# Kernel tuning notes

Measured on AMD Instinct MI355X. Metric: run time of the kernel, lower is better.

Reference implementation:

```python
import jax, jax.numpy as jnp
import numpy as np

T, B, IN_DIM, H = 4096, 2048, 1, 10  # len(input), seq_length, input_dim, hidden_dim


def setup_inputs() -> dict:
    key = jax.random.key(0)
    ks = jax.random.split(key, 11)
    s_in = 1.0 / np.sqrt(H)  # torch LSTM/Linear init scale
    u = lambda k, shape: jax.random.uniform(k, shape, jnp.float32, -s_in, s_in)
    return {
        "x": jax.random.normal(ks[0], (T, B, IN_DIM), jnp.float32),
        # layer 0 (input_size=1), layer 1 (input_size=H); torch gate order i,f,g,o
        "W_ih0": u(ks[1], (4 * H, IN_DIM)),
        "W_hh0": u(ks[2], (4 * H, H)),
        "b_ih0": u(ks[3], (4 * H,)),
        "b_hh0": u(ks[4], (4 * H,)),
        "W_ih1": u(ks[5], (4 * H, H)),
        "W_hh1": u(ks[6], (4 * H, H)),
        "b_ih1": u(ks[7], (4 * H,)),
        "b_hh1": u(ks[8], (4 * H,)),
        "W_lin": u(ks[9], (1, H)),
        "b_lin": u(ks[10], (1,)),
    }


def _lstm_layer(x, W_ih, W_hh, b_ih, b_hh):
    # x: (T, B, in); precompute input contributions for all timesteps at once
    xw = jnp.einsum("tbi,gi->tbg", x, W_ih) + b_ih + b_hh  # (T, B, 4H)
    Whh_T = W_hh.T

    def step(carry, xt):
        h, c = carry
        gates = xt + h @ Whh_T  # (B, 4H)
        i, f, g, o = jnp.split(gates, 4, axis=-1)
        i = jax.nn.sigmoid(i)
        f = jax.nn.sigmoid(f)
        g = jnp.tanh(g)
        o = jax.nn.sigmoid(o)
        c = f * c + i * g
        h = o * jnp.tanh(c)
        return (h, c), h

    b = x.shape[1]
    h0 = jnp.zeros((b, W_hh.shape[1]), x.dtype)
    _, hs = jax.lax.scan(step, (h0, h0), xw)
    return hs  # (T, B, H)


def reference(x, W_ih0, W_hh0, b_ih0, b_hh0, W_ih1, W_hh1, b_ih1, b_hh1, W_lin, b_lin):
    h1 = _lstm_layer(x, W_ih0, W_hh0, b_ih0, b_hh0)   # (T, B, H)
    h2 = _lstm_layer(h1, W_ih1, W_hh1, b_ih1, b_hh1)  # (T, B, H)
    # faithful to original: view(seq_length, len(input), H)[-1] is a raw reshape
    last = h2.reshape(B, T, H)[-1]                    # (T, H)
    return last @ W_lin.T + b_lin                     # (T, 1)
```

## Files before the change

### kernel.cpp

```cpp
#include <hip/hip_runtime.h>

namespace {

constexpr int T_STEPS = 4096;
constexpr int NBATCH  = 2048;
constexpr int HID     = 10;
constexpr float L2E   = 1.4426950408889634f;

typedef float v2f __attribute__((ext_vector_type(2)));
typedef float v4f __attribute__((ext_vector_type(4)));

__device__ __forceinline__ float ex2(float x){ return __builtin_amdgcn_exp2f(x); }
__device__ __forceinline__ float rcp_(float x){ return __builtin_amdgcn_rcpf(x); }

template<int IMM>
__device__ __forceinline__ float swz(float v){
    return __int_as_float(__builtin_amdgcn_ds_swizzle(__float_as_int(v), IMM));
}
__device__ __forceinline__ float bperm(int addr, float v){
    return __int_as_float(__builtin_amdgcn_ds_bpermute(addr, __float_as_int(v)));
}
template<int CTRL>
__device__ __forceinline__ float dpp(float v){
    return __int_as_float(__builtin_amdgcn_update_dpp(0, __float_as_int(v), CTRL, 0xF, 0xF, true));
}
__device__ __forceinline__ void pk_fma(v2f &a, v2f b, v2f c){
    asm("v_pk_fma_f32 %0, %1, %2, %0" : "+v"(a) : "v"(b), "v"(c));
}


__device__ __forceinline__ void lstm_step(
    const v2f (&Wp)[2][5], float wx0, float wx1, float b0, float b1,
    float selA, float kA, float kB,
    float* hwp, const char* rdb,
    float &hn, float &c, float xv,
    float wlin, float blin, int t_l1, float* __restrict__ out, int b)
{
    *hwp = hn;
    asm volatile("" ::: "memory");
    const v4f Va = *(const v4f*)(rdb);
    const v4f Vb = *(const v4f*)(rdb+16);
    const v2f Vc = *(const v2f*)(rdb+32);
    const v2f va01 = __builtin_shufflevector(Va, Va, 0, 1);
    const v2f va23 = __builtin_shufflevector(Va, Va, 2, 3);
    const v2f vb01 = __builtin_shufflevector(Vb, Vb, 0, 1);
    const v2f vb23 = __builtin_shufflevector(Vb, Vb, 2, 3);

    v2f A0 = { fmaf(wx0, xv, b0), 0.0f };
    v2f A1 = { fmaf(wx1, xv, b1), 0.0f };
    pk_fma(A0, Wp[0][0], va01);  pk_fma(A1, Wp[1][0], va01);
    pk_fma(A0, Wp[0][1], va23);  pk_fma(A1, Wp[1][1], va23);
    pk_fma(A0, Wp[0][2], vb01);  pk_fma(A1, Wp[1][2], vb01);
    pk_fma(A0, Wp[0][3], vb23);  pk_fma(A1, Wp[1][3], vb23);
    pk_fma(A0, Wp[0][4], Vc);    pk_fma(A1, Wp[1][4], Vc);
    float a0 = A0.x + A0.y;
    float a1 = A1.x + A1.y;

    a0 = fmaf(selA, dpp<0x108>(a0), a0);
    a1 = fmaf(selA, dpp<0x108>(a1), a1);

    const float r0 = rcp_(1.0f + ex2(a0));
    const float r1 = rcp_(1.0f + ex2(a1));
    const float g0 = fmaf(kA, r0, kB);
    const float g1 = r1;

    const float gv = dpp<0x101>(g0);
    const float ov = dpp<0x101>(g1);
    c = fmaf(g1, c, g0 * gv);
    const float tc = fmaf(-2.0f, rcp_(1.0f + ex2(c * (2.0f*L2E))), 1.0f);
    hn = ov * tc;

    if (t_l1 >= T_STEPS-2) {
        float p = hn * wlin;
        p += swz<0x041F>(p); p += swz<0x081F>(p); p += swz<0x101F>(p);
        p += swz<0x201F>(p); p += swz<0x401F>(p);
        p += bperm((((int)threadIdx.x ^ 32) & 63)*4, p);
        if (threadIdx.x == 0)
            out[(t_l1 - (T_STEPS-2))*NBATCH + b] = p + blin;
    }
}

__device__ __forceinline__ float rdlane(float v, int lane){
    return __int_as_float(__builtin_amdgcn_readlane(__float_as_int(v), lane));
}

__global__ __launch_bounds__(64) void lstm2_kernel(
    const float* __restrict__ x,
    const float* __restrict__ Wih0, const float* __restrict__ Whh0,
    const float* __restrict__ bih0, const float* __restrict__ bhh0,
    const float* __restrict__ Wih1, const float* __restrict__ Whh1,
    const float* __restrict__ bih1, const float* __restrict__ bhh1,
    const float* __restrict__ Wlin, const float* __restrict__ blin_p,
    float* __restrict__ out)
{
    __shared__ float hx[96];

    const int tid = (int)threadIdx.x;
    const int b   = (int)blockIdx.x;

    int role, q;
    if      (tid < 16){ role=0; q=tid; }
    else if (tid < 24){ role=1; q=tid-16; }
    else if (tid < 32){ role=2; q=tid-24; }
    else if (tid < 40){ role=1; q=tid-32+8; }
    else if (tid < 48){ role=2; q=tid-40+8; }
    else if (tid < 52){ role=1; q=tid-48+16; }
    else if (tid < 56){ role=0; q=tid-52+16; }
    else if (tid < 60){ role=2; q=tid-56+16; }
    else              { role=3; q=0; }
    const int h = q >> 1, p = q & 1;
    const int gate0 = p ? 2 : 0, gate1 = p ? 3 : 1;
    const float s0 = (gate0 == 2) ? 2.0f*L2E : -L2E;
    const float s1 = -L2E;

    float W0[HID], W1[HID], wx0=0.0f, wx1=0.0f, b0=0.0f, b1=0.0f;
    const int r0i = gate0*HID + h, r1i = gate1*HID + h;
    if (role == 0){
        #pragma unroll
        for (int j=0;j<HID;++j){ W0[j]=Whh0[r0i*HID+j]*s0; W1[j]=Whh0[r1i*HID+j]*s1; }
        wx0 = Wih0[r0i]*s0;  wx1 = Wih0[r1i]*s1;
        b0 = (bih0[r0i]+bhh0[r0i])*s0;  b1 = (bih0[r1i]+bhh0[r1i])*s1;
    } else if (role == 1){
        #pragma unroll
        for (int j=0;j<HID;++j){ W0[j]=Wih1[r0i*HID+j]*s0; W1[j]=Wih1[r1i*HID+j]*s1; }
        b0 = (bih1[r0i]+bhh1[r0i])*s0;  b1 = (bih1[r1i]+bhh1[r1i])*s1;
    } else if (role == 2){
        #pragma unroll
        for (int j=0;j<HID;++j){ W0[j]=Whh1[r0i*HID+j]*s0; W1[j]=Whh1[r1i*HID+j]*s1; }
    } else {
        #pragma unroll
        for (int j=0;j<HID;++j){ W0[j]=0.0f; W1[j]=0.0f; }
    }
    v2f Wp[2][5];
    #pragma unroll
    for (int k=0;k<5;++k){ Wp[0][k]=v2f{W0[2*k],W0[2*k+1]}; Wp[1][k]=v2f{W1[2*k],W1[2*k+1]}; }

    const float selA = (role==1) ? 1.0f : 0.0f;
    const float kA = p ? -2.0f : 1.0f;
    const float kB = p ?  1.0f : 0.0f;
    const bool owner = (p==0) && (role==0 || role==1);
    const int wslot = owner ? (role==0 ? h : 12+h) : (24+tid);
    float* hwp = &hx[wslot];
    const char* rdb = (const char*)hx + (role==2 ? 48 : 0);
    const float wlin = (role==1 && p==0) ? Wlin[h] : 0.0f;
    const float blin = blin_p[0];

    float hn = 0.0f, c = 0.0f;

    const float* xp = x + (size_t)(tid & 7) * NBATCH + b;
    float xpre = xp[0];

    {
        const float zb0 = (role==0) ? b0 : 0.0f, zb1 = (role==0) ? b1 : 0.0f;
        lstm_step(Wp, wx0,wx1, zb0,zb1, selA,kA,kB, hwp,rdb, hn,c, rdlane(xpre,0), wlin,blin, -1, out, b);
        lstm_step(Wp, wx0,wx1, b0,b1, selA,kA,kB, hwp,rdb, hn,c, rdlane(xpre,1), wlin,blin, 0, out, b);
        lstm_step(Wp, wx0,wx1, b0,b1, selA,kA,kB, hwp,rdb, hn,c, rdlane(xpre,2), wlin,blin, 1, out, b);
        lstm_step(Wp, wx0,wx1, b0,b1, selA,kA,kB, hwp,rdb, hn,c, rdlane(xpre,3), wlin,blin, 2, out, b);
        lstm_step(Wp, wx0,wx1, b0,b1, selA,kA,kB, hwp,rdb, hn,c, rdlane(xpre,4), wlin,blin, 3, out, b);
        lstm_step(Wp, wx0,wx1, b0,b1, selA,kA,kB, hwp,rdb, hn,c, rdlane(xpre,5), wlin,blin, 4, out, b);
        lstm_step(Wp, wx0,wx1, b0,b1, selA,kA,kB, hwp,rdb, hn,c, rdlane(xpre,6), wlin,blin, 5, out, b);
        lstm_step(Wp, wx0,wx1, b0,b1, selA,kA,kB, hwp,rdb, hn,c, rdlane(xpre,7), wlin,blin, 6, out, b);
    }

    for (int i=1; i<512; ++i){
        const float xcur = xp[(size_t)i*8*NBATCH];
        const int s0b = i*8;
        lstm_step(Wp, wx0,wx1, b0,b1, selA,kA,kB, hwp,rdb, hn,c, rdlane(xcur,0), wlin,blin, s0b-1, out, b);
        lstm_step(Wp, wx0,wx1, b0,b1, selA,kA,kB, hwp,rdb, hn,c, rdlane(xcur,1), wlin,blin, s0b+0, out, b);
        lstm_step(Wp, wx0,wx1, b0,b1, selA,kA,kB, hwp,rdb, hn,c, rdlane(xcur,2), wlin,blin, s0b+1, out, b);
        lstm_step(Wp, wx0,wx1, b0,b1, selA,kA,kB, hwp,rdb, hn,c, rdlane(xcur,3), wlin,blin, s0b+2, out, b);
        lstm_step(Wp, wx0,wx1, b0,b1, selA,kA,kB, hwp,rdb, hn,c, rdlane(xcur,4), wlin,blin, s0b+3, out, b);
        lstm_step(Wp, wx0,wx1, b0,b1, selA,kA,kB, hwp,rdb, hn,c, rdlane(xcur,5), wlin,blin, s0b+4, out, b);
        lstm_step(Wp, wx0,wx1, b0,b1, selA,kA,kB, hwp,rdb, hn,c, rdlane(xcur,6), wlin,blin, s0b+5, out, b);
        lstm_step(Wp, wx0,wx1, b0,b1, selA,kA,kB, hwp,rdb, hn,c, rdlane(xcur,7), wlin,blin, s0b+6, out, b);
    }

    lstm_step(Wp, wx0,wx1, b0,b1, selA,kA,kB, hwp,rdb, hn,c, 0.0f, wlin,blin, T_STEPS-1, out, b);
}

}

extern "C" void kernel_launch(void* const* d_in, const int* in_sizes, int n_in,
                              void* d_out, int out_size, void* d_ws, size_t ws_size,
                              hipStream_t stream) {
    const float* x    = (const float*)d_in[0];
    const float* Wih0 = (const float*)d_in[1];
    const float* Whh0 = (const float*)d_in[2];
    const float* bih0 = (const float*)d_in[3];
    const float* bhh0 = (const float*)d_in[4];
    const float* Wih1 = (const float*)d_in[5];
    const float* Whh1 = (const float*)d_in[6];
    const float* bih1 = (const float*)d_in[7];
    const float* bhh1 = (const float*)d_in[8];
    const float* Wlin = (const float*)d_in[9];
    const float* blin = (const float*)d_in[10];
    float* out = (float*)d_out;

    hipLaunchKernelGGL(lstm2_kernel, dim3(NBATCH), dim3(64), 0, stream,
                       x, Wih0, Whh0, bih0, bhh0, Wih1, Whh1, bih1, bhh1, Wlin, blin, out);
}
```

Before: 901.0 us.

## Double-buffer LDS hidden-state exchange and prefetch next x chunk one iteration ahead

Each step now writes its new hidden state into the LDS buffer that the following step reads, instead of writing the previous step's state at the start of the step. Even and odd steps alternate between two buffers, so the store can come right after the state is computed. This moves the LDS write off the front of each step's critical path and removes the read-after-write ordering within a step. The x input for the next group of 8 steps is also loaded one loop iteration early, hiding global-load latency. The cost is more LDS, an explicit zero-init of both buffers, and one extra live register.

```diff
diff --git a/kernel.cpp b/kernel.cpp
--- a/kernel.cpp
+++ b/kernel.cpp
@@ -26,6 +26,9 @@
 }
 __device__ __forceinline__ void pk_fma(v2f &a, v2f b, v2f c){
     asm("v_pk_fma_f32 %0, %1, %2, %0" : "+v"(a) : "v"(b), "v"(c));
+}
+__device__ __forceinline__ float rdlane(float v, int lane){
+    return __int_as_float(__builtin_amdgcn_readlane(__float_as_int(v), lane));
 }
 
 
@@ -36,8 +39,6 @@
     float &hn, float &c, float xv,
     float wlin, float blin, int t_l1, float* __restrict__ out, int b)
 {
-    *hwp = hn;
-    asm volatile("" ::: "memory");
     const v4f Va = *(const v4f*)(rdb);
     const v4f Vb = *(const v4f*)(rdb+16);
     const v2f Vc = *(const v2f*)(rdb+32);
@@ -70,6 +71,9 @@
     const float tc = fmaf(-2.0f, rcp_(1.0f + ex2(c * (2.0f*L2E))), 1.0f);
     hn = ov * tc;
 
+    *hwp = hn;
+    asm volatile("" ::: "memory");
+
     if (t_l1 >= T_STEPS-2) {
         float p = hn * wlin;
         p += swz<0x041F>(p); p += swz<0x081F>(p); p += swz<0x101F>(p);
@@ -78,10 +82,6 @@
         if (threadIdx.x == 0)
             out[(t_l1 - (T_STEPS-2))*NBATCH + b] = p + blin;
     }
-}
-
-__device__ __forceinline__ float rdlane(float v, int lane){
-    return __int_as_float(__builtin_amdgcn_readlane(__float_as_int(v), lane));
 }
 
 __global__ __launch_bounds__(64) void lstm2_kernel(
@@ -93,7 +93,7 @@
     const float* __restrict__ Wlin, const float* __restrict__ blin_p,
     float* __restrict__ out)
 {
-    __shared__ float hx[96];
+    __shared__ __attribute__((aligned(16))) float hx[128];
 
     const int tid = (int)threadIdx.x;
     const int b   = (int)blockIdx.x;
@@ -139,43 +139,52 @@
     const float kA = p ? -2.0f : 1.0f;
     const float kB = p ?  1.0f : 0.0f;
     const bool owner = (p==0) && (role==0 || role==1);
-    const int wslot = owner ? (role==0 ? h : 12+h) : (24+tid);
-    float* hwp = &hx[wslot];
-    const char* rdb = (const char*)hx + (role==2 ? 48 : 0);
+    const int slot = owner ? (role==0 ? h : 12+h) : -1;
+
+    float* hwpE = &hx[slot >= 0 ? 24+slot : 48+tid];
+    float* hwpO = &hx[slot >= 0 ?    slot : 48+tid];
+    const char* rdbE = (const char*)hx + (role==2 ? 48 : 0);
+    const char* rdbO = (const char*)hx + 96 + (role==2 ? 48 : 0);
     const float wlin = (role==1 && p==0) ? Wlin[h] : 0.0f;
     const float blin = blin_p[0];
 
+    hx[slot >= 0 ? slot : 48+tid] = 0.0f;
+    hx[slot >= 0 ? 24+slot : 48+tid] = 0.0f;
+    asm volatile("" ::: "memory");
+
     float hn = 0.0f, c = 0.0f;
 
     const float* xp = x + (size_t)(tid & 7) * NBATCH + b;
-    float xpre = xp[0];
+    float xcur = xp[0];
+    float xnxt = xp[(size_t)8 * NBATCH];
 
     {
         const float zb0 = (role==0) ? b0 : 0.0f, zb1 = (role==0) ? b1 : 0.0f;
-        lstm_step(Wp, wx0,wx1, zb0,zb1, selA,kA,kB, hwp,rdb, hn,c, rdlane(xpre,0), wlin,blin, -1, out, b);
-        lstm_step(Wp, wx0,wx1, b0,b1, selA,kA,kB, hwp,rdb, hn,c, rdlane(xpre,1), wlin,blin, 0, out, b);
-        lstm_step(Wp, wx0,wx1, b0,b1, selA,kA,kB, hwp,rdb, hn,c, rdlane(xpre,2), wlin,blin, 1, out, b);
-        lstm_step(Wp, wx0,wx1, b0,b1, selA,kA,kB, hwp,rdb, hn,c, rdlane(xpre,3), wlin,blin, 2, out, b);
-        lstm_step(Wp, wx0,wx1, b0,b1, selA,kA,kB, hwp,rdb, hn,c, rdlane(xpre,4), wlin,blin, 3, out, b);
-        lstm_step(Wp, wx0,wx1, b0,b1, selA,kA,kB, hwp,rdb, hn,c, rdlane(xpre,5), wlin,blin, 4, out, b);
-        lstm_step(Wp, wx0,wx1, b0,b1, selA,kA,kB, hwp,rdb, hn,c, rdlane(xpre,6), wlin,blin, 5, out, b);
-        lstm_step(Wp, wx0,wx1, b0,b1, selA,kA,kB, hwp,rdb, hn,c, rdlane(xpre,7), wlin,blin, 6, out, b);
+        lstm_step(Wp, wx0,wx1, zb0,zb1, selA,kA,kB, hwpE,rdbE, hn,c, rdlane(xcur,0), wlin,blin, -1, out, b);
+        lstm_step(Wp, wx0,wx1, b0,b1, selA,kA,kB, hwpO,rdbO, hn,c, rdlane(xcur,1), wlin,blin, 0, out, b);
+        lstm_step(Wp, wx0,wx1, b0,b1, selA,kA,kB, hwpE,rdbE, hn,c, rdlane(xcur,2), wlin,blin, 1, out, b);
+        lstm_step(Wp, wx0,wx1, b0,b1, selA,kA,kB, hwpO,rdbO, hn,c, rdlane(xcur,3), wlin,blin, 2, out, b);
+        lstm_step(Wp, wx0,wx1, b0,b1, selA,kA,kB, hwpE,rdbE, hn,c, rdlane(xcur,4), wlin,blin, 3, out, b);
+        lstm_step(Wp, wx0,wx1, b0,b1, selA,kA,kB, hwpO,rdbO, hn,c, rdlane(xcur,5), wlin,blin, 4, out, b);
+        lstm_step(Wp, wx0,wx1, b0,b1, selA,kA,kB, hwpE,rdbE, hn,c, rdlane(xcur,6), wlin,blin, 5, out, b);
+        lstm_step(Wp, wx0,wx1, b0,b1, selA,kA,kB, hwpO,rdbO, hn,c, rdlane(xcur,7), wlin,blin, 6, out, b);
     }
 
     for (int i=1; i<512; ++i){
-        const float xcur = xp[(size_t)i*8*NBATCH];
+        xcur = xnxt;
+        if (i < 511) xnxt = xp[(size_t)(i+1)*8*NBATCH];
         const int s0b = i*8;
-        lstm_step(Wp, wx0,wx1, b0,b1, selA,kA,kB, hwp,rdb, hn,c, rdlane(xcur,0), wlin,blin, s0b-1, out, b);
-        lstm_step(Wp, wx0,wx1, b0,b1, selA,kA,kB, hwp,rdb, hn,c, rdlane(xcur,1), wlin,blin, s0b+0, out, b);
-        lstm_step(Wp, wx0,wx1, b0,b1, selA,kA,kB, hwp,rdb, hn,c, rdlane(xcur,2), wlin,blin, s0b+1, out, b);
-        lstm_step(Wp, wx0,wx1, b0,b1, selA,kA,kB, hwp,rdb, hn,c, rdlane(xcur,3), wlin,blin, s0b+2, out, b);
-        lstm_step(Wp, wx0,wx1, b0,b1, selA,kA,kB, hwp,rdb, hn,c, rdlane(xcur,4), wlin,blin, s0b+3, out, b);
-        lstm_step(Wp, wx0,wx1, b0,b1, selA,kA,kB, hwp,rdb, hn,c, rdlane(xcur,5), wlin,blin, s0b+4, out, b);
-        lstm_step(Wp, wx0,wx1, b0,b1, selA,kA,kB, hwp,rdb, hn,c, rdlane(xcur,6), wlin,blin, s0b+5, out, b);
-        lstm_step(Wp, wx0,wx1, b0,b1, selA,kA,kB, hwp,rdb, hn,c, rdlane(xcur,7), wlin,blin, s0b+6, out, b);
-    }
-
-    lstm_step(Wp, wx0,wx1, b0,b1, selA,kA,kB, hwp,rdb, hn,c, 0.0f, wlin,blin, T_STEPS-1, out, b);
+        lstm_step(Wp, wx0,wx1, b0,b1, selA,kA,kB, hwpE,rdbE, hn,c, rdlane(xcur,0), wlin,blin, s0b-1, out, b);
+        lstm_step(Wp, wx0,wx1, b0,b1, selA,kA,kB, hwpO,rdbO, hn,c, rdlane(xcur,1), wlin,blin, s0b+0, out, b);
+        lstm_step(Wp, wx0,wx1, b0,b1, selA,kA,kB, hwpE,rdbE, hn,c, rdlane(xcur,2), wlin,blin, s0b+1, out, b);
+        lstm_step(Wp, wx0,wx1, b0,b1, selA,kA,kB, hwpO,rdbO, hn,c, rdlane(xcur,3), wlin,blin, s0b+2, out, b);
+        lstm_step(Wp, wx0,wx1, b0,b1, selA,kA,kB, hwpE,rdbE, hn,c, rdlane(xcur,4), wlin,blin, s0b+3, out, b);
+        lstm_step(Wp, wx0,wx1, b0,b1, selA,kA,kB, hwpO,rdbO, hn,c, rdlane(xcur,5), wlin,blin, s0b+4, out, b);
+        lstm_step(Wp, wx0,wx1, b0,b1, selA,kA,kB, hwpE,rdbE, hn,c, rdlane(xcur,6), wlin,blin, s0b+5, out, b);
+        lstm_step(Wp, wx0,wx1, b0,b1, selA,kA,kB, hwpO,rdbO, hn,c, rdlane(xcur,7), wlin,blin, s0b+6, out, b);
+    }
+
+    lstm_step(Wp, wx0,wx1, b0,b1, selA,kA,kB, hwpE,rdbE, hn,c, 0.0f, wlin,blin, T_STEPS-1, out, b);
 }
 
 }
```

After: 817.3 us. 9.3% less time.

## Restructure LSTM step: LDS exchange at step end, shared reciprocal, x prefetch

Applied to the files above, without the earlier changes.

Each step now writes the new hidden state to LDS and reads the neighbours' values at the end of the step, carrying them in registers into the next step. Four other changes come with it. The two sigmoid reciprocals are merged into one rcp of the product of the denominators. The x load is software-prefetched one 8-step block ahead. The output-reduction branch becomes a compile-time template flag. Non-owner write slots move to avoid overlapping the read window, and LDS is aligned and enlarged. These changes aim to shorten the serial dependency chain per timestep, at the risk of a small precision change from the combined reciprocal.

```diff
diff --git a/kernel.cpp b/kernel.cpp
--- a/kernel.cpp
+++ b/kernel.cpp
@@ -27,24 +27,25 @@
 __device__ __forceinline__ void pk_fma(v2f &a, v2f b, v2f c){
     asm("v_pk_fma_f32 %0, %1, %2, %0" : "+v"(a) : "v"(b), "v"(c));
 }
-
-
+__device__ __forceinline__ float rdlane(float v, int lane){
+    return __int_as_float(__builtin_amdgcn_readlane(__float_as_int(v), lane));
+}
+
+
+template<bool OUT>
 __device__ __forceinline__ void lstm_step(
     const v2f (&Wp)[2][5], float wx0, float wx1, float b0, float b1,
     float selA, float kA, float kB,
     float* hwp, const char* rdb,
+    v4f &Va, v4f &Vb, v2f &Vc,
     float &hn, float &c, float xv,
-    float wlin, float blin, int t_l1, float* __restrict__ out, int b)
+    float wlin, float blin, int t_l1, float* out, int b)
 {
-    *hwp = hn;
-    asm volatile("" ::: "memory");
-    const v4f Va = *(const v4f*)(rdb);
-    const v4f Vb = *(const v4f*)(rdb+16);
-    const v2f Vc = *(const v2f*)(rdb+32);
     const v2f va01 = __builtin_shufflevector(Va, Va, 0, 1);
     const v2f va23 = __builtin_shufflevector(Va, Va, 2, 3);
     const v2f vb01 = __builtin_shufflevector(Vb, Vb, 0, 1);
     const v2f vb23 = __builtin_shufflevector(Vb, Vb, 2, 3);
+    const v2f vc01 = Vc;
 
     v2f A0 = { fmaf(wx0, xv, b0), 0.0f };
     v2f A1 = { fmaf(wx1, xv, b1), 0.0f };
@@ -52,15 +53,18 @@
     pk_fma(A0, Wp[0][1], va23);  pk_fma(A1, Wp[1][1], va23);
     pk_fma(A0, Wp[0][2], vb01);  pk_fma(A1, Wp[1][2], vb01);
     pk_fma(A0, Wp[0][3], vb23);  pk_fma(A1, Wp[1][3], vb23);
-    pk_fma(A0, Wp[0][4], Vc);    pk_fma(A1, Wp[1][4], Vc);
+    pk_fma(A0, Wp[0][4], vc01);  pk_fma(A1, Wp[1][4], vc01);
     float a0 = A0.x + A0.y;
     float a1 = A1.x + A1.y;
 
     a0 = fmaf(selA, dpp<0x108>(a0), a0);
     a1 = fmaf(selA, dpp<0x108>(a1), a1);
 
-    const float r0 = rcp_(1.0f + ex2(a0));
-    const float r1 = rcp_(1.0f + ex2(a1));
+    const float e0 = ex2(a0), e1 = ex2(a1);
+    const float d0 = 1.0f + e0, d1 = 1.0f + e1;
+    const float rD = rcp_(d0 * d1);
+    const float r0 = d1 * rD;
+    const float r1 = d0 * rD;
     const float g0 = fmaf(kA, r0, kB);
     const float g1 = r1;
 
@@ -70,7 +74,13 @@
     const float tc = fmaf(-2.0f, rcp_(1.0f + ex2(c * (2.0f*L2E))), 1.0f);
     hn = ov * tc;
 
-    if (t_l1 >= T_STEPS-2) {
+    *hwp = hn;
+    asm volatile("" ::: "memory");
+    Va = *(const v4f*)(rdb);
+    Vb = *(const v4f*)(rdb+16);
+    Vc = *(const v2f*)(rdb+32);
+
+    if (OUT) {
         float p = hn * wlin;
         p += swz<0x041F>(p); p += swz<0x081F>(p); p += swz<0x101F>(p);
         p += swz<0x201F>(p); p += swz<0x401F>(p);
@@ -78,10 +88,6 @@
         if (threadIdx.x == 0)
             out[(t_l1 - (T_STEPS-2))*NBATCH + b] = p + blin;
     }
-}
-
-__device__ __forceinline__ float rdlane(float v, int lane){
-    return __int_as_float(__builtin_amdgcn_readlane(__float_as_int(v), lane));
 }
 
 __global__ __launch_bounds__(64) void lstm2_kernel(
@@ -93,7 +99,7 @@
     const float* __restrict__ Wlin, const float* __restrict__ blin_p,
     float* __restrict__ out)
 {
-    __shared__ float hx[96];
+    __shared__ __attribute__((aligned(16))) float hx[112];
 
     const int tid = (int)threadIdx.x;
     const int b   = (int)blockIdx.x;
@@ -139,43 +145,58 @@
     const float kA = p ? -2.0f : 1.0f;
     const float kB = p ?  1.0f : 0.0f;
     const bool owner = (p==0) && (role==0 || role==1);
-    const int wslot = owner ? (role==0 ? h : 12+h) : (24+tid);
+    const int wslot = owner ? (role==0 ? h : 12+h) : (48+tid);
     float* hwp = &hx[wslot];
     const char* rdb = (const char*)hx + (role==2 ? 48 : 0);
     const float wlin = (role==1 && p==0) ? Wlin[h] : 0.0f;
     const float blin = blin_p[0];
 
     float hn = 0.0f, c = 0.0f;
+    v4f Va = {0,0,0,0}, Vb = {0,0,0,0};
+    v2f Vc = {0,0};
 
     const float* xp = x + (size_t)(tid & 7) * NBATCH + b;
-    float xpre = xp[0];
+    float xcur = xp[0];
+    float xnxt = xp[(size_t)8 * NBATCH];
 
     {
         const float zb0 = (role==0) ? b0 : 0.0f, zb1 = (role==0) ? b1 : 0.0f;
-        lstm_step(Wp, wx0,wx1, zb0,zb1, selA,kA,kB, hwp,rdb, hn,c, rdlane(xpre,0), wlin,blin, -1, out, b);
-        lstm_step(Wp, wx0,wx1, b0,b1, selA,kA,kB, hwp,rdb, hn,c, rdlane(xpre,1), wlin,blin, 0, out, b);
-        lstm_step(Wp, wx0,wx1, b0,b1, selA,kA,kB, hwp,rdb, hn,c, rdlane(xpre,2), wlin,blin, 1, out, b);
-        lstm_step(Wp, wx0,wx1, b0,b1, selA,kA,kB, hwp,rdb, hn,c, rdlane(xpre,3), wlin,blin, 2, out, b);
-        lstm_step(Wp, wx0,wx1, b0,b1, selA,kA,kB, hwp,rdb, hn,c, rdlane(xpre,4), wlin,blin, 3, out, b);
-        lstm_step(Wp, wx0,wx1, b0,b1, selA,kA,kB, hwp,rdb, hn,c, rdlane(xpre,5), wlin,blin, 4, out, b);
-        lstm_step(Wp, wx0,wx1, b0,b1, selA,kA,kB, hwp,rdb, hn,c, rdlane(xpre,6), wlin,blin, 5, out, b);
-        lstm_step(Wp, wx0,wx1, b0,b1, selA,kA,kB, hwp,rdb, hn,c, rdlane(xpre,7), wlin,blin, 6, out, b);
-    }
-
-    for (int i=1; i<512; ++i){
-        const float xcur = xp[(size_t)i*8*NBATCH];
-        const int s0b = i*8;
-        lstm_step(Wp, wx0,wx1, b0,b1, selA,kA,kB, hwp,rdb, hn,c, rdlane(xcur,0), wlin,blin, s0b-1, out, b);
-        lstm_step(Wp, wx0,wx1, b0,b1, selA,kA,kB, hwp,rdb, hn,c, rdlane(xcur,1), wlin,blin, s0b+0, out, b);
-        lstm_step(Wp, wx0,wx1, b0,b1, selA,kA,kB, hwp,rdb, hn,c, rdlane(xcur,2), wlin,blin, s0b+1, out, b);
-        lstm_step(Wp, wx0,wx1, b0,b1, selA,kA,kB, hwp,rdb, hn,c, rdlane(xcur,3), wlin,blin, s0b+2, out, b);
-        lstm_step(Wp, wx0,wx1, b0,b1, selA,kA,kB, hwp,rdb, hn,c, rdlane(xcur,4), wlin,blin, s0b+3, out, b);
-        lstm_step(Wp, wx0,wx1, b0,b1, selA,kA,kB, hwp,rdb, hn,c, rdlane(xcur,5), wlin,blin, s0b+4, out, b);
-        lstm_step(Wp, wx0,wx1, b0,b1, selA,kA,kB, hwp,rdb, hn,c, rdlane(xcur,6), wlin,blin, s0b+5, out, b);
-        lstm_step(Wp, wx0,wx1, b0,b1, selA,kA,kB, hwp,rdb, hn,c, rdlane(xcur,7), wlin,blin, s0b+6, out, b);
-    }
-
-    lstm_step(Wp, wx0,wx1, b0,b1, selA,kA,kB, hwp,rdb, hn,c, 0.0f, wlin,blin, T_STEPS-1, out, b);
+        lstm_step<false>(Wp, wx0,wx1, zb0,zb1, selA,kA,kB, hwp,rdb, Va,Vb,Vc, hn,c, rdlane(xcur,0), wlin,blin, 0, out, b);
+        lstm_step<false>(Wp, wx0,wx1, b0,b1, selA,kA,kB, hwp,rdb, Va,Vb,Vc, hn,c, rdlane(xcur,1), wlin,blin, 0, out, b);
+        lstm_step<false>(Wp, wx0,wx1, b0,b1, selA,kA,kB, hwp,rdb, Va,Vb,Vc, hn,c, rdlane(xcur,2), wlin,blin, 0, out, b);
+        lstm_step<false>(Wp, wx0,wx1, b0,b1, selA,kA,kB, hwp,rdb, Va,Vb,Vc, hn,c, rdlane(xcur,3), wlin,blin, 0, out, b);
+        lstm_step<false>(Wp, wx0,wx1, b0,b1, selA,kA,kB, hwp,rdb, Va,Vb,Vc, hn,c, rdlane(xcur,4), wlin,blin, 0, out, b);
+        lstm_step<false>(Wp, wx0,wx1, b0,b1, selA,kA,kB, hwp,rdb, Va,Vb,Vc, hn,c, rdlane(xcur,5), wlin,blin, 0, out, b);
+        lstm_step<false>(Wp, wx0,wx1, b0,b1, selA,kA,kB, hwp,rdb, Va,Vb,Vc, hn,c, rdlane(xcur,6), wlin,blin, 0, out, b);
+        lstm_step<false>(Wp, wx0,wx1, b0,b1, selA,kA,kB, hwp,rdb, Va,Vb,Vc, hn,c, rdlane(xcur,7), wlin,blin, 0, out, b);
+    }
+
+    for (int i=1; i<511; ++i){
+        xcur = xnxt;
+        xnxt = xp[(size_t)(i+1)*8*NBATCH];
+        lstm_step<false>(Wp, wx0,wx1, b0,b1, selA,kA,kB, hwp,rdb, Va,Vb,Vc, hn,c, rdlane(xcur,0), wlin,blin, 0, out, b);
+        lstm_step<false>(Wp, wx0,wx1, b0,b1, selA,kA,kB, hwp,rdb, Va,Vb,Vc, hn,c, rdlane(xcur,1), wlin,blin, 0, out, b);
+        lstm_step<false>(Wp, wx0,wx1, b0,b1, selA,kA,kB, hwp,rdb, Va,Vb,Vc, hn,c, rdlane(xcur,2), wlin,blin, 0, out, b);
+        lstm_step<false>(Wp, wx0,wx1, b0,b1, selA,kA,kB, hwp,rdb, Va,Vb,Vc, hn,c, rdlane(xcur,3), wlin,blin, 0, out, b);
+        lstm_step<false>(Wp, wx0,wx1, b0,b1, selA,kA,kB, hwp,rdb, Va,Vb,Vc, hn,c, rdlane(xcur,4), wlin,blin, 0, out, b);
+        lstm_step<false>(Wp, wx0,wx1, b0,b1, selA,kA,kB, hwp,rdb, Va,Vb,Vc, hn,c, rdlane(xcur,5), wlin,blin, 0, out, b);
+        lstm_step<false>(Wp, wx0,wx1, b0,b1, selA,kA,kB, hwp,rdb, Va,Vb,Vc, hn,c, rdlane(xcur,6), wlin,blin, 0, out, b);
+        lstm_step<false>(Wp, wx0,wx1, b0,b1, selA,kA,kB, hwp,rdb, Va,Vb,Vc, hn,c, rdlane(xcur,7), wlin,blin, 0, out, b);
+    }
+
+    {
+        xcur = xnxt;
+        lstm_step<false>(Wp, wx0,wx1, b0,b1, selA,kA,kB, hwp,rdb, Va,Vb,Vc, hn,c, rdlane(xcur,0), wlin,blin, 0, out, b);
+        lstm_step<false>(Wp, wx0,wx1, b0,b1, selA,kA,kB, hwp,rdb, Va,Vb,Vc, hn,c, rdlane(xcur,1), wlin,blin, 0, out, b);
+        lstm_step<false>(Wp, wx0,wx1, b0,b1, selA,kA,kB, hwp,rdb, Va,Vb,Vc, hn,c, rdlane(xcur,2), wlin,blin, 0, out, b);
+        lstm_step<false>(Wp, wx0,wx1, b0,b1, selA,kA,kB, hwp,rdb, Va,Vb,Vc, hn,c, rdlane(xcur,3), wlin,blin, 0, out, b);
+        lstm_step<false>(Wp, wx0,wx1, b0,b1, selA,kA,kB, hwp,rdb, Va,Vb,Vc, hn,c, rdlane(xcur,4), wlin,blin, 0, out, b);
+        lstm_step<false>(Wp, wx0,wx1, b0,b1, selA,kA,kB, hwp,rdb, Va,Vb,Vc, hn,c, rdlane(xcur,5), wlin,blin, 0, out, b);
+        lstm_step<false>(Wp, wx0,wx1, b0,b1, selA,kA,kB, hwp,rdb, Va,Vb,Vc, hn,c, rdlane(xcur,6), wlin,blin, 0, out, b);
+        lstm_step<true >(Wp, wx0,wx1, b0,b1, selA,kA,kB, hwp,rdb, Va,Vb,Vc, hn,c, rdlane(xcur,7), wlin,blin, T_STEPS-2, out, b);
+    }
+
+    lstm_step<true>(Wp, wx0,wx1, b0,b1, selA,kA,kB, hwp,rdb, Va,Vb,Vc, hn,c, 0.0f, wlin,blin, T_STEPS-1, out, b);
 }
 
 }
```

After: 829.5 us. -7.9%, faster.
